# Performance work log

Measured on AMD Instinct MI355X. Metric: run time of the kernel, lower is better.

Reference implementation:

```python
import jax, jax.numpy as jnp
import numpy as np

D = 1024      # model_dim
H = 16        # num_attention_heads
HD = D // H   # head dim
FFN = 4096    # ffn_dim
EPS = 1e-5


def _mha(q_in, k_in, v_in, wq, bq, wk, bk, wv, bv):
    B, Sq, _ = q_in.shape
    Sk = k_in.shape[1]
    def split(x, S):
        return x.reshape(B, S, H, HD).transpose(0, 2, 1, 3)  # [B,H,S,HD]
    Q = split(q_in @ wq + bq, Sq)
    K = split(k_in @ wk + bk, Sk)
    V = split(v_in @ wv + bv, Sk)
    scores = jnp.einsum('bhqd,bhkd->bhqk', Q, K) / (HD ** 0.5)
    probs = jax.nn.softmax(scores, axis=-1)
    ctx = jnp.einsum('bhqk,bhkd->bhqd', probs, V)
    return ctx.transpose(0, 2, 1, 3).reshape(B, Sq, D)


def _ln(x, g, b):
    mu = jnp.mean(x, axis=-1, keepdims=True)
    var = jnp.mean(jnp.square(x - mu), axis=-1, keepdims=True)
    return (x - mu) * jax.lax.rsqrt(var + EPS) * g + b


def setup_inputs() -> dict:
    key = jax.random.key(0)
    ks = jax.random.split(key, 24)
    s = 1.0 / np.sqrt(D)
    inp = {
        'hidden_states': jax.random.normal(ks[0], (2, 2048, D), jnp.float32),
        'encoder_hidden_states': jax.random.normal(ks[1], (2, 2048, D), jnp.float32),
        # self-attention projections
        'sa_wq': jax.random.normal(ks[2], (D, D), jnp.float32) * s,
        'sa_bq': jnp.zeros((D,), jnp.float32),
        'sa_wk': jax.random.normal(ks[3], (D, D), jnp.float32) * s,
        'sa_bk': jnp.zeros((D,), jnp.float32),
        'sa_wv': jax.random.normal(ks[4], (D, D), jnp.float32) * s,
        'sa_bv': jnp.zeros((D,), jnp.float32),
        'ln1_g': jnp.ones((D,), jnp.float32),
        'ln1_b': jnp.zeros((D,), jnp.float32),
        # cross-attention projections
        'ca_wq': jax.random.normal(ks[5], (D, D), jnp.float32) * s,
        'ca_bq': jnp.zeros((D,), jnp.float32),
        'ca_wk': jax.random.normal(ks[6], (D, D), jnp.float32) * s,
        'ca_bk': jnp.zeros((D,), jnp.float32),
        'ca_wv': jax.random.normal(ks[7], (D, D), jnp.float32) * s,
        'ca_bv': jnp.zeros((D,), jnp.float32),
        'ln2_g': jnp.ones((D,), jnp.float32),
        'ln2_b': jnp.zeros((D,), jnp.float32),
        # feed-forward
        'fc1_w': jax.random.normal(ks[8], (D, FFN), jnp.float32) * s,
        'fc1_b': jnp.zeros((FFN,), jnp.float32),
        'fc2_w': jax.random.normal(ks[9], (FFN, D), jnp.float32) * (1.0 / np.sqrt(FFN)),
        'fc2_b': jnp.zeros((D,), jnp.float32),
        'ln3_g': jnp.ones((D,), jnp.float32),
        'ln3_b': jnp.zeros((D,), jnp.float32),
    }
    return inp


def reference(hidden_states, encoder_hidden_states,
              sa_wq, sa_bq, sa_wk, sa_bk, sa_wv, sa_bv, ln1_g, ln1_b,
              ca_wq, ca_bq, ca_wk, ca_bk, ca_wv, ca_bv, ln2_g, ln2_b,
              fc1_w, fc1_b, fc2_w, fc2_b, ln3_g, ln3_b):
    # self-attention + residual + LN  (dropout = identity in eval)
    h = _mha(hidden_states, hidden_states, hidden_states,
             sa_wq, sa_bq, sa_wk, sa_bk, sa_wv, sa_bv)
    x = _ln(hidden_states + h, ln1_g, ln1_b)
    # cross-attention + residual + LN
    h = _mha(x, encoder_hidden_states, encoder_hidden_states,
             ca_wq, ca_bq, ca_wk, ca_bk, ca_wv, ca_bv)
    x = _ln(x + h, ln2_g, ln2_b)
    # feed-forward + residual + LN
    h = jax.nn.relu(x @ fc1_w + fc1_b) @ fc2_w + fc2_b
    return _ln(x + h, ln3_g, ln3_b)
```

## Files before the change

kernel.cpp:

```cpp
#include <hip/hip_runtime.h>


typedef unsigned short u16;
typedef unsigned int u32;
typedef short v8s __attribute__((ext_vector_type(8)));
typedef float v4f __attribute__((ext_vector_type(4)));

#define LDP 72
#define LOG2E 1.44269504088896340736f

__device__ __forceinline__ float b2f(u16 h) {
    return __uint_as_float(((u32)h) << 16);
}
__device__ __forceinline__ u16 f2b(float f) {
    u32 u = __float_as_uint(f);
    u += 0x7fffu + ((u >> 16) & 1u);
    return (u16)(u >> 16);
}
__device__ __forceinline__ u32 pack2_rz(float lo, float hi) {
    return (__float_as_uint(hi) & 0xffff0000u) | (__float_as_uint(lo) >> 16);
}
__device__ __forceinline__ void gload16(const void* g, void* l) {
    __builtin_amdgcn_global_load_lds(
        (const __attribute__((address_space(1))) unsigned int*)g,
        (__attribute__((address_space(3))) unsigned int*)l, 16, 0, 0);
}
__device__ __forceinline__ int xcd_swz(int orig, int nwg) {
    const int q = nwg >> 3, r = nwg & 7;
    const int xcd = orig & 7, idx = orig >> 3;
    return (xcd < r ? xcd * (q + 1) : r * (q + 1) + (xcd - r) * q) + idx;
}

__global__ __launch_bounds__(256) void conv_f2b(
    const float* __restrict__ src, u16* __restrict__ dst)
{
    const size_t i = ((size_t)blockIdx.x * 256 + threadIdx.x) * 8;
    float4 a = *(const float4*)&src[i];
    float4 b = *(const float4*)&src[i + 4];
    ushort4 o0, o1;
    o0.x = f2b(a.x); o0.y = f2b(a.y); o0.z = f2b(a.z); o0.w = f2b(a.w);
    o1.x = f2b(b.x); o1.y = f2b(b.y); o1.z = f2b(b.z); o1.w = f2b(b.w);
    *(ushort4*)&dst[i] = o0;
    *(ushort4*)&dst[i + 4] = o1;
}

__global__ __launch_bounds__(256) void transpose_f2b(
    const float* __restrict__ src, u16* __restrict__ dst, int R, int C)
{
    __shared__ u16 tile[32][33];
    const int t  = threadIdx.x;
    const int tx = t & 31, ty = t >> 5;
    const int r0 = blockIdx.y * 32, c0 = blockIdx.x * 32;
#pragma unroll
    for (int i = 0; i < 32; i += 8)
        tile[ty + i][tx] = f2b(src[(size_t)(r0 + ty + i) * C + c0 + tx]);
    __syncthreads();
#pragma unroll
    for (int i = 0; i < 32; i += 8)
        dst[(size_t)(c0 + ty + i) * R + r0 + tx] = tile[tx][ty + i];
}

__global__ __launch_bounds__(256) void prep_bias(
    const float* __restrict__ bq, const float* __restrict__ bk, const float* __restrict__ bv,
    const float* __restrict__ cbk, const float* __restrict__ cbv,
    float* __restrict__ sab, float* __restrict__ cakvb)
{
    int i = blockIdx.x * 256 + threadIdx.x;
    if (i < 1024) {
        sab[i]          = bq[i];
        sab[1024 + i]   = bk[i];
        sab[2048 + i]   = bv[i];
        cakvb[i]        = cbk[i];
        cakvb[1024 + i] = cbv[i];
    }
}

template <int BM, int BN>
__global__ __launch_bounds__(256) void gemm_bt(
    const u16* __restrict__ A, const u16* __restrict__ Bt,
    const float* __restrict__ bias, u16* __restrict__ C,
    int M, int N, int K, int relu, int qcols, float qscale,
    u16* __restrict__ vt, int vtcol0)
{
    constexpr int MI = BM / 32;
    constexpr int NI = BN / 32;
    __shared__ __align__(16) u16 Al[BM * 64];
    __shared__ __align__(16) u16 Bl[BN * 64];
    const int tid  = threadIdx.x;
    const int wave = tid >> 6, lane = tid & 63;
    const int quad = lane >> 4, tl = lane & 15;
    const int nwg  = gridDim.x * gridDim.y;
    const int wgid = xcd_swz(blockIdx.y * gridDim.x + blockIdx.x, nwg);
    const int bx   = wgid % gridDim.x, by = wgid / gridDim.x;
    const int bm0 = by * BM, bn0 = bx * BN;
    const int wm = (wave >> 1) * (BM / 2), wn = (wave & 1) * (BN / 2);
    const int srow = lane >> 3;
    const int scol = (((lane & 7) ^ srow) << 3);

    const v4f z4 = {0.f, 0.f, 0.f, 0.f};
    v4f acc[MI][NI];
#pragma unroll
    for (int i = 0; i < MI; ++i)
#pragma unroll
        for (int j = 0; j < NI; ++j) acc[i][j] = z4;

    for (int kt = 0; kt < K; kt += 64) {
#pragma unroll
        for (int i = 0; i < MI; ++i) {
            const int c = wave * MI + i;
            const int row = c * 8 + srow;
            gload16(&A[(size_t)(bm0 + row) * K + kt + scol], &Al[c * 512]);
        }
#pragma unroll
        for (int i = 0; i < NI; ++i) {
            const int c = wave * NI + i;
            const int row = c * 8 + srow;
            gload16(&Bt[(size_t)(bn0 + row) * K + kt + scol], &Bl[c * 512]);
        }
        __syncthreads();
#pragma unroll
        for (int kk = 0; kk < 2; ++kk) {
            const int pc = ((kk * 4 + quad) ^ (tl & 7)) << 3;
            v8s af[MI], bf[NI];
#pragma unroll
            for (int i = 0; i < MI; ++i) af[i] = *(const v8s*)&Al[(wm + i * 16 + tl) * 64 + pc];
#pragma unroll
            for (int i = 0; i < NI; ++i) bf[i] = *(const v8s*)&Bl[(wn + i * 16 + tl) * 64 + pc];
#pragma unroll
            for (int mi = 0; mi < MI; ++mi)
#pragma unroll
                for (int ni = 0; ni < NI; ++ni)
                    acc[mi][ni] = __builtin_amdgcn_mfma_f32_16x16x32_bf16(
                        af[mi], bf[ni], acc[mi][ni], 0, 0, 0);
        }
        __syncthreads();
    }
#pragma unroll
    for (int ni = 0; ni < NI; ++ni) {
        int col = bn0 + wn + ni * 16 + tl;
        float bv = bias[col];
        if (vtcol0 >= 0 && col >= vtcol0) {
            int cv = col - vtcol0;
            int h = cv >> 6, hd = cv & 63;
#pragma unroll
            for (int mi = 0; mi < MI; ++mi) {
                int row0 = bm0 + wm + mi * 16 + (quad << 2);
                int bb = row0 >> 11, s = row0 & 2047;
                ushort4 pk;
                pk.x = f2b(acc[mi][ni][0] + bv);
                pk.y = f2b(acc[mi][ni][1] + bv);
                pk.z = f2b(acc[mi][ni][2] + bv);
                pk.w = f2b(acc[mi][ni][3] + bv);
                *(ushort4*)&vt[((size_t)(bb * 16 + h) * 64 + hd) * 2048 + s] = pk;
            }
        } else {
            float sc = (col < qcols) ? qscale : 1.0f;
#pragma unroll
            for (int mi = 0; mi < MI; ++mi) {
                int row0 = bm0 + wm + mi * 16 + (quad << 2);
#pragma unroll
                for (int r = 0; r < 4; ++r) {
                    float vv = acc[mi][ni][r] + bv;
                    if (relu) vv = fmaxf(vv, 0.f);
                    vv *= sc;
                    C[(size_t)(row0 + r) * N + col] = f2b(vv);
                }
            }
        }
    }
}

__global__ __launch_bounds__(512) void attn_v7(
    const u16* __restrict__ Q, int qs, const u16* __restrict__ Kp, int ks,
    const u16* __restrict__ Vt, u16* __restrict__ O, int os, int Sk)
{
    __shared__ __align__(16) u16 Kl[128 * 64];
    __shared__ __align__(16) u16 Vtl[64 * 128];
    __shared__ __align__(16) u16 Pl[8][16 * LDP];

    const int tid  = threadIdx.x;
    const int wave = tid >> 6, lane = tid & 63;
    const int quad = lane >> 4, tl = lane & 15;
    const int nwg  = gridDim.x * gridDim.y;
    const int wgid = xcd_swz(blockIdx.y * gridDim.x + blockIdx.x, nwg);
    const int bx   = wgid % gridDim.x, by = wgid / gridDim.x;
    const int b = by >> 4, h = by & 15;
    const int srow = lane >> 3;
    const int scolK = (((lane & 7) ^ srow) << 3);
    const int vri = lane >> 4, vj = lane & 15;

    const u16* qb  = Q  + (size_t)(b * 2048) * qs + h * 64;
    const u16* kb  = Kp + (size_t)(b * 2048) * ks + h * 64;
    const u16* vtb = Vt + (size_t)by * 64 * 2048;
    u16*       ob  = O  + (size_t)(b * 2048) * os + h * 64;
    const int qr0 = bx * 128 + wave * 16;

    v8s qf[2];
#pragma unroll
    for (int kk = 0; kk < 2; ++kk)
        qf[kk] = *(const v8s*)&qb[(size_t)(qr0 + tl) * qs + kk * 32 + quad * 8];

    const v4f z4 = {0.f, 0.f, 0.f, 0.f};
    v4f oacc[4] = {z4, z4, z4, z4};
    float l_q = 0.f;
    u16* Pw = &Pl[wave][0];

    const int pc0 = (quad ^ (tl & 7)) << 3;
    const int pc1 = ((4 + quad) ^ (tl & 7)) << 3;

    for (int kt = 0; kt < Sk; kt += 128) {
#pragma unroll
        for (int i = 0; i < 2; ++i) {
            const int c = wave * 2 + i;
            const int row = c * 8 + srow;
            gload16(&kb[(size_t)(kt + row) * ks + scolK], &Kl[c * 512]);
        }
#pragma unroll
        for (int i = 0; i < 2; ++i) {
            const int c = wave * 2 + i;
            const int vr = c * 4 + vri;
            const int g = (vj & 8) | ((vj & 7) ^ (vr & 7));
            gload16(&vtb[(size_t)vr * 2048 + kt + (g << 3)], &Vtl[c * 512]);
        }
        __syncthreads();

#pragma unroll
        for (int hf = 0; hf < 2; ++hf) {
#pragma unroll
            for (int nt = 0; nt < 4; ++nt) {
                const int krow = ((hf * 4 + nt) * 16 + tl) * 64;
                v8s k0 = *(const v8s*)&Kl[krow + pc0];
                v8s k1 = *(const v8s*)&Kl[krow + pc1];
                v4f a = z4;
                a = __builtin_amdgcn_mfma_f32_16x16x32_bf16(k0, qf[0], a, 0, 0, 0);
                a = __builtin_amdgcn_mfma_f32_16x16x32_bf16(k1, qf[1], a, 0, 0, 0);
                float p0 = __builtin_amdgcn_exp2f(a[0]);
                float p1 = __builtin_amdgcn_exp2f(a[1]);
                float p2 = __builtin_amdgcn_exp2f(a[2]);
                float p3 = __builtin_amdgcn_exp2f(a[3]);
                l_q += (p0 + p1) + (p2 + p3);
                uint2 pk;
                pk.x = pack2_rz(p0, p1);
                pk.y = pack2_rz(p2, p3);
                *(uint2*)&Pw[tl * LDP + nt * 16 + quad * 4] = pk;
            }
            asm volatile("" ::: "memory");

            v8s pf0 = *(const v8s*)&Pw[tl * LDP + quad * 8];
            v8s pf1 = *(const v8s*)&Pw[tl * LDP + 32 + quad * 8];
            const int pv0 = ((hf * 8) | (quad ^ (tl & 7))) << 3;
            const int pv1 = ((hf * 8) | ((4 + quad) ^ (tl & 7))) << 3;
            __builtin_amdgcn_s_setprio(1);
#pragma unroll
            for (int d = 0; d < 4; ++d) {
                const int vbase = (d * 16 + tl) * 128;
                v8s v0 = *(const v8s*)&Vtl[vbase + pv0];
                v8s v1 = *(const v8s*)&Vtl[vbase + pv1];
                oacc[d] = __builtin_amdgcn_mfma_f32_16x16x32_bf16(pf0, v0, oacc[d], 0, 0, 0);
                oacc[d] = __builtin_amdgcn_mfma_f32_16x16x32_bf16(pf1, v1, oacc[d], 0, 0, 0);
            }
            __builtin_amdgcn_s_setprio(0);
            asm volatile("" ::: "memory");
        }
        __syncthreads();
    }

    l_q += __shfl_xor(l_q, 16);
    l_q += __shfl_xor(l_q, 32);

#pragma unroll
    for (int r = 0; r < 4; ++r) {
        float inv = 1.0f / __shfl(l_q, quad * 4 + r);
#pragma unroll
        for (int d = 0; d < 4; ++d)
            ob[(size_t)(qr0 + quad * 4 + r) * os + d * 16 + tl] =
                f2b(oacc[d][r] * inv);
    }
}

template <int XF32, int OF32>
__global__ __launch_bounds__(256) void add_ln(
    const void* __restrict__ Xv, const u16* __restrict__ Hh,
    const float* __restrict__ G, const float* __restrict__ Bb,
    void* __restrict__ Outv)
{
    const int row = blockIdx.x, t = threadIdx.x;
    float v0, v1, v2, v3;
    {
        ushort4 hv = *(const ushort4*)&Hh[(size_t)row * 1024 + t * 4];
        if (XF32) {
            const float* xr = (const float*)Xv + (size_t)row * 1024;
            float4 xv = *(const float4*)&xr[t * 4];
            v0 = xv.x + b2f(hv.x); v1 = xv.y + b2f(hv.y);
            v2 = xv.z + b2f(hv.z); v3 = xv.w + b2f(hv.w);
        } else {
            const u16* xr = (const u16*)Xv + (size_t)row * 1024;
            ushort4 xv = *(const ushort4*)&xr[t * 4];
            v0 = b2f(xv.x) + b2f(hv.x); v1 = b2f(xv.y) + b2f(hv.y);
            v2 = b2f(xv.z) + b2f(hv.z); v3 = b2f(xv.w) + b2f(hv.w);
        }
    }

    float s1 = v0 + v1 + v2 + v3;
    float s2 = v0 * v0 + v1 * v1 + v2 * v2 + v3 * v3;
#pragma unroll
    for (int o = 1; o < 64; o <<= 1) {
        s1 += __shfl_xor(s1, o);
        s2 += __shfl_xor(s2, o);
    }
    __shared__ float red[8];
    const int wave = t >> 6, lane = t & 63;
    if (lane == 0) { red[wave] = s1; red[4 + wave] = s2; }
    __syncthreads();
    s1 = red[0] + red[1] + red[2] + red[3];
    s2 = red[4] + red[5] + red[6] + red[7];

    const float mu = s1 * (1.f / 1024.f);
    float var = s2 * (1.f / 1024.f) - mu * mu;
    var = fmaxf(var, 0.f);
    const float rs = rsqrtf(var + 1e-5f);

    float4 gv = *(const float4*)&G[t * 4];
    float4 bv = *(const float4*)&Bb[t * 4];
    float o0 = (v0 - mu) * rs * gv.x + bv.x;
    float o1 = (v1 - mu) * rs * gv.y + bv.y;
    float o2 = (v2 - mu) * rs * gv.z + bv.z;
    float o3 = (v3 - mu) * rs * gv.w + bv.w;

    if (OF32) {
        float4 ov = {o0, o1, o2, o3};
        *(float4*)&((float*)Outv)[(size_t)row * 1024 + t * 4] = ov;
    } else {
        ushort4 ov;
        ov.x = f2b(o0); ov.y = f2b(o1); ov.z = f2b(o2); ov.w = f2b(o3);
        *(ushort4*)&((u16*)Outv)[(size_t)row * 1024 + t * 4] = ov;
    }
}

extern "C" void kernel_launch(void* const* d_in, const int* in_sizes, int n_in,
                              void* d_out, int out_size, void* d_ws, size_t ws_size,
                              hipStream_t stream) {
    const float* x0  = (const float*)d_in[0];
    const float* enc = (const float*)d_in[1];

    char* wsb = (char*)d_ws;
    const size_t MB = 1024u * 1024u;
    u16*   wt_sa   = (u16*)(wsb);
    u16*   wt_caq  = (u16*)(wsb + 6  * MB);
    u16*   wt_cakv = (u16*)(wsb + 8  * MB);
    float* sab     = (float*)(wsb + 12 * MB);
    float* cakvb   = (float*)(wsb + 12 * MB + 16384);
    char*  arena   = wsb + 12 * MB + 32768;
    u16* QKV    = (u16*)(arena);
    u16* hbuf   = (u16*)(arena + 24 * MB);
    u16* x0b    = (u16*)(arena + 24 * MB);
    u16* encb   = (u16*)(arena + 24 * MB);
    u16* x1     = (u16*)(arena + 32 * MB);
    u16* Vt     = (u16*)(arena + 40 * MB);
    u16* Q2     = (u16*)(arena);
    u16* KV2    = (u16*)(arena + 8  * MB);
    u16* x2     = (u16*)(arena);
    u16* wt_fc1 = (u16*)(wsb);
    u16* wt_fc2 = (u16*)(arena + 8  * MB);
    u16* tbuf   = (u16*)(arena + 16 * MB);
    u16* h3     = (u16*)(wsb);

    const float QSC = 0.125f * LOG2E;

    prep_bias<<<4, 256, 0, stream>>>(
        (const float*)d_in[3], (const float*)d_in[5], (const float*)d_in[7],
        (const float*)d_in[13], (const float*)d_in[15], sab, cakvb);

    transpose_f2b<<<dim3(32, 32), 256, 0, stream>>>((const float*)d_in[2],  wt_sa,               1024, 1024);
    transpose_f2b<<<dim3(32, 32), 256, 0, stream>>>((const float*)d_in[4],  wt_sa + 1024*1024,   1024, 1024);
    transpose_f2b<<<dim3(32, 32), 256, 0, stream>>>((const float*)d_in[6],  wt_sa + 2*1024*1024, 1024, 1024);
    transpose_f2b<<<dim3(32, 32), 256, 0, stream>>>((const float*)d_in[10], wt_caq,              1024, 1024);
    transpose_f2b<<<dim3(32, 32), 256, 0, stream>>>((const float*)d_in[12], wt_cakv,             1024, 1024);
    transpose_f2b<<<dim3(32, 32), 256, 0, stream>>>((const float*)d_in[14], wt_cakv + 1024*1024, 1024, 1024);

    conv_f2b<<<2048, 256, 0, stream>>>(x0, x0b);
    gemm_bt<128, 128><<<dim3(24, 32), 256, 0, stream>>>(
        x0b, wt_sa, sab, QKV, 4096, 3072, 1024, 0, 1024, QSC, Vt, 2048);
    attn_v7<<<dim3(16, 32), 512, 0, stream>>>(QKV, 3072, QKV + 1024, 3072, Vt, hbuf, 1024, 2048);
    add_ln<1, 0><<<4096, 256, 0, stream>>>(x0, hbuf, (const float*)d_in[8], (const float*)d_in[9], x1);

    conv_f2b<<<2048, 256, 0, stream>>>(enc, encb);
    gemm_bt<64, 64><<<dim3(16, 64), 256, 0, stream>>>(
        x1, wt_caq, (const float*)d_in[11], Q2, 4096, 1024, 1024, 0, 1024, QSC, (u16*)nullptr, -1);
    gemm_bt<64, 128><<<dim3(16, 64), 256, 0, stream>>>(
        encb, wt_cakv, cakvb, KV2, 4096, 2048, 1024, 0, 0, 1.0f, Vt, 1024);
    attn_v7<<<dim3(16, 32), 512, 0, stream>>>(Q2, 1024, KV2, 2048, Vt, hbuf, 1024, 2048);
    add_ln<0, 0><<<4096, 256, 0, stream>>>(x1, hbuf, (const float*)d_in[16], (const float*)d_in[17], x2);

    transpose_f2b<<<dim3(128, 32), 256, 0, stream>>>((const float*)d_in[18], wt_fc1, 1024, 4096);
    transpose_f2b<<<dim3(32, 128), 256, 0, stream>>>((const float*)d_in[20], wt_fc2, 4096, 1024);
    gemm_bt<128, 128><<<dim3(32, 32), 256, 0, stream>>>(
        x2, wt_fc1, (const float*)d_in[19], tbuf, 4096, 4096, 1024, 1, 0, 1.0f, (u16*)nullptr, -1);
    gemm_bt<64, 64><<<dim3(16, 64), 256, 0, stream>>>(
        tbuf, wt_fc2, (const float*)d_in[21], h3, 4096, 1024, 4096, 0, 0, 1.0f, (u16*)nullptr, -1);
    add_ln<0, 1><<<4096, 256, 0, stream>>>(x2, h3, (const float*)d_in[22], (const float*)d_in[23], d_out);
}
```

Baseline: 474.2 us.

## Double-buffer K tiles and register-prefetch V tiles in attention kernel

```diff
diff --git a/kernel.cpp b/kernel.cpp
--- a/kernel.cpp
+++ b/kernel.cpp
@@ -170,11 +170,11 @@
     }
 }
 
-__global__ __launch_bounds__(512) void attn_v7(
+__global__ __launch_bounds__(512) void attn_v9(
     const u16* __restrict__ Q, int qs, const u16* __restrict__ Kp, int ks,
     const u16* __restrict__ Vt, u16* __restrict__ O, int os, int Sk)
 {
-    __shared__ __align__(16) u16 Kl[128 * 64];
+    __shared__ __align__(16) u16 Kl[2][128 * 64];
     __shared__ __align__(16) u16 Vtl[64 * 128];
     __shared__ __align__(16) u16 Pl[8][16 * LDP];
 
@@ -208,29 +208,53 @@
     const int pc0 = (quad ^ (tl & 7)) << 3;
     const int pc1 = ((4 + quad) ^ (tl & 7)) << 3;
 
+#pragma unroll
+    for (int i = 0; i < 2; ++i) {
+        const int c = wave * 2 + i;
+        gload16(&kb[(size_t)(c * 8 + srow) * ks + scolK], &Kl[0][c * 512]);
+    }
+#pragma unroll
+    for (int i = 0; i < 2; ++i) {
+        const int c = wave * 2 + i;
+        const int vr = c * 4 + vri;
+        const int g = (vj & 8) | ((vj & 7) ^ (vr & 7));
+        gload16(&vtb[(size_t)vr * 2048 + (g << 3)], &Vtl[c * 512]);
+    }
+    __syncthreads();
+
+    int cur = 0;
     for (int kt = 0; kt < Sk; kt += 128) {
-#pragma unroll
-        for (int i = 0; i < 2; ++i) {
-            const int c = wave * 2 + i;
-            const int row = c * 8 + srow;
-            gload16(&kb[(size_t)(kt + row) * ks + scolK], &Kl[c * 512]);
-        }
-#pragma unroll
-        for (int i = 0; i < 2; ++i) {
-            const int c = wave * 2 + i;
-            const int vr = c * 4 + vri;
-            const int g = (vj & 8) | ((vj & 7) ^ (vr & 7));
-            gload16(&vtb[(size_t)vr * 2048 + kt + (g << 3)], &Vtl[c * 512]);
-        }
-        __syncthreads();
+        const int more = (kt + 128 < Sk) ? 1 : 0;
+        v8s vp0, vp1;
+        if (more) {
+            {
+                const int c = wave * 2 + 0;
+                const int vr = c * 4 + vri;
+                const int g = (vj & 8) | ((vj & 7) ^ (vr & 7));
+                vp0 = *(const v8s*)&vtb[(size_t)vr * 2048 + kt + 128 + (g << 3)];
+            }
+            {
+                const int c = wave * 2 + 1;
+                const int vr = c * 4 + vri;
+                const int g = (vj & 8) | ((vj & 7) ^ (vr & 7));
+                vp1 = *(const v8s*)&vtb[(size_t)vr * 2048 + kt + 128 + (g << 3)];
+            }
+#pragma unroll
+            for (int i = 0; i < 2; ++i) {
+                const int c = wave * 2 + i;
+                const int row = c * 8 + srow;
+                gload16(&kb[(size_t)(kt + 128 + row) * ks + scolK], &Kl[cur ^ 1][c * 512]);
+            }
+        }
+        const u16* Kc = &Kl[cur][0];
 
 #pragma unroll
         for (int hf = 0; hf < 2; ++hf) {
 #pragma unroll
             for (int nt = 0; nt < 4; ++nt) {
                 const int krow = ((hf * 4 + nt) * 16 + tl) * 64;
-                v8s k0 = *(const v8s*)&Kl[krow + pc0];
-                v8s k1 = *(const v8s*)&Kl[krow + pc1];
+                v8s k0 = *(const v8s*)&Kc[krow + pc0];
+                v8s k1 = *(const v8s*)&Kc[krow + pc1];
                 v4f a = z4;
                 a = __builtin_amdgcn_mfma_f32_16x16x32_bf16(k0, qf[0], a, 0, 0, 0);
                 a = __builtin_amdgcn_mfma_f32_16x16x32_bf16(k1, qf[1], a, 0, 0, 0);
@@ -262,7 +286,14 @@
             __builtin_amdgcn_s_setprio(0);
             asm volatile("" ::: "memory");
         }
+
         __syncthreads();
+        if (more) {
+            *(v8s*)&Vtl[(wave * 2 + 0) * 512 + lane * 8] = vp0;
+            *(v8s*)&Vtl[(wave * 2 + 1) * 512 + lane * 8] = vp1;
+        }
+        __syncthreads();
+        cur ^= 1;
     }
 
     l_q += __shfl_xor(l_q, 16);
@@ -381,7 +412,7 @@
     conv_f2b<<<2048, 256, 0, stream>>>(x0, x0b);
     gemm_bt<128, 128><<<dim3(24, 32), 256, 0, stream>>>(
         x0b, wt_sa, sab, QKV, 4096, 3072, 1024, 0, 1024, QSC, Vt, 2048);
-    attn_v7<<<dim3(16, 32), 512, 0, stream>>>(QKV, 3072, QKV + 1024, 3072, Vt, hbuf, 1024, 2048);
+    attn_v9<<<dim3(16, 32), 512, 0, stream>>>(QKV, 3072, QKV + 1024, 3072, Vt, hbuf, 1024, 2048);
     add_ln<1, 0><<<4096, 256, 0, stream>>>(x0, hbuf, (const float*)d_in[8], (const float*)d_in[9], x1);
 
     conv_f2b<<<2048, 256, 0, stream>>>(enc, encb);
@@ -389,7 +420,7 @@
         x1, wt_caq, (const float*)d_in[11], Q2, 4096, 1024, 1024, 0, 1024, QSC, (u16*)nullptr, -1);
     gemm_bt<64, 128><<<dim3(16, 64), 256, 0, stream>>>(
         encb, wt_cakv, cakvb, KV2, 4096, 2048, 1024, 0, 0, 1.0f, Vt, 1024);
-    attn_v7<<<dim3(16, 32), 512, 0, stream>>>(Q2, 1024, KV2, 2048, Vt, hbuf, 1024, 2048);
+    attn_v9<<<dim3(16, 32), 512, 0, stream>>>(Q2, 1024, KV2, 2048, Vt, hbuf, 1024, 2048);
     add_ln<0, 0><<<4096, 256, 0, stream>>>(x1, hbuf, (const float*)d_in[16], (const float*)d_in[17], x2);
 
     transpose_f2b<<<dim3(128, 32), 256, 0, stream>>>((const float*)d_in[18], wt_fc1, 1024, 4096);
```

Result: slower. 492.6 us (+3.9%).
